# Performance work log

Hardware: AMD Instinct MI355X
Metric: run time of the kernel (lower is better)

## Reference

```python
import jax, jax.numpy as jnp
import numpy as np

B, C, H, W = 4, 2048, 32, 32


def conv1x1(x, Wt, b):
    # 1x1 conv == per-pixel matmul over channels
    return jnp.einsum('oc,bchw->bohw', Wt, x) + b[None, :, None, None]


def cross_attention(Q, K, V):
    b, c, h, w = Q.shape
    q = Q.reshape(b, c, h * w)   # [B, C, N]
    k = K.reshape(b, c, h * w)
    v = V.reshape(b, c, h * w)
    scores = jnp.einsum('bcn,bcm->bnm', q, k) / jnp.sqrt(jnp.asarray(c, jnp.float32))
    attn = jax.nn.softmax(scores, axis=-1)          # [B, N, N]
    out = jnp.einsum('bcm,bnm->bcn', v, attn)       # V @ attn^T
    return out.reshape(b, c, h, w)


def setup_inputs() -> dict:
    key = jax.random.key(0)
    ks = jax.random.split(key, 14)
    d = {
        'F_rgb': jax.random.normal(ks[0], (B, C, H, W), jnp.float32),
        'F_indices': jax.random.normal(ks[1], (B, C, H, W), jnp.float32),
    }
    names = ['q_rgb', 'k_rgb', 'v_rgb', 'q_ind', 'k_ind', 'v_ind']
    for i, n in enumerate(names):
        d['W_' + n] = jax.random.normal(ks[2 + 2 * i], (C, C), jnp.float32) * 0.02
        d['b_' + n] = jax.random.normal(ks[3 + 2 * i], (C,), jnp.float32) * 0.01
    return d


def reference(F_rgb, F_indices, W_q_rgb, b_q_rgb, W_k_rgb, b_k_rgb, W_v_rgb, b_v_rgb,
              W_q_ind, b_q_ind, W_k_ind, b_k_ind, W_v_ind, b_v_ind):
    # RGB queries attend over index features
    Q_rgb = conv1x1(F_rgb, W_q_rgb, b_q_rgb)
    K_ind = conv1x1(F_indices, W_k_ind, b_k_ind)
    V_ind = conv1x1(F_indices, W_v_ind, b_v_ind)
    F_rgb_attended = cross_attention(Q_rgb, K_ind, V_ind)
    # Index queries attend over RGB features
    Q_ind = conv1x1(F_indices, W_q_ind, b_q_ind)
    K_rgb = conv1x1(F_rgb, W_k_rgb, b_k_rgb)
    V_rgb = conv1x1(F_rgb, W_v_rgb, b_v_rgb)
    F_ind_attended = cross_attention(Q_ind, K_rgb, V_rgb)
    F_final = F_rgb_attended + F_ind_attended
    attention_weights = jnp.stack([F_rgb_attended, F_ind_attended], axis=1)  # [B,2,C,H,W]
    # pre_attention_outputs is an identity passthrough of the inputs
    return (F_final, F_rgb, F_indices, attention_weights)
```

## Files before the change

kernel.cpp:

```cpp
#include <hip/hip_runtime.h>

typedef __bf16 bf16x8 __attribute__((ext_vector_type(8)));
typedef float  f32x4  __attribute__((ext_vector_type(4)));
typedef unsigned short u16;
typedef unsigned short u16x8 __attribute__((ext_vector_type(8)));

__device__ __forceinline__ u16 f2bf(float f) {
  unsigned u = __builtin_bit_cast(unsigned, f);
  u += 0x7fffu + ((u >> 16) & 1u);
  return (u16)(u >> 16);
}
__device__ __forceinline__ float bf2f(u16 h) {
  return __builtin_bit_cast(float, (unsigned)h << 16);
}

using gvoid = __attribute__((address_space(1))) void;
using svoid = __attribute__((address_space(3))) void;
__device__ __forceinline__ void load_lds16(const void* g, void* s) {
  __builtin_amdgcn_global_load_lds((const gvoid*)g, (svoid*)s, 16, 0, 0);
}

__global__ void prep(const float* __restrict__ Fr, const float* __restrict__ Fi,
                     u16* __restrict__ FTr, u16* __restrict__ FTi,
                     float* __restrict__ Or, float* __restrict__ Oi,
                     const float* __restrict__ s0, const float* __restrict__ s1,
                     const float* __restrict__ s2, const float* __restrict__ s3,
                     const float* __restrict__ s4, const float* __restrict__ s5,
                     u16* __restrict__ Wall) {
  const int tx = threadIdx.x, ty = threadIdx.y;
  const int t2 = ty * 32 + tx;
  if (blockIdx.z >= 8) {
    const int gi = (blockIdx.z - 8) * 1024 + blockIdx.y * 32 + blockIdx.x;
    const int chunk = gi >> 12;
    const int i = (gi & 4095) * 256 + t2;
    const float* src;
    switch (chunk) {
      case 0: src = s0; break; case 1: src = s1; break; case 2: src = s2; break;
      case 3: src = s3; break; case 4: src = s4; break; default: src = s5; break;
    }
    float4 v = ((const float4*)src)[i];
    ushort4 o;
    o.x = f2bf(v.x); o.y = f2bf(v.y); o.z = f2bf(v.z); o.w = f2bf(v.w);
    ((ushort4*)(Wall + (long)chunk * 4194304))[i] = o;
    return;
  }
  __shared__ float tile[64][33];
  const int b = blockIdx.z & 3;
  const bool ind = (blockIdx.z >= 4);
  const float* F = ind ? Fi : Fr;
  u16* FT = ind ? FTi : FTr;
  float* O = ind ? Oi : Or;
  const int n0 = blockIdx.x * 32, c0 = blockIdx.y * 64;
  const long boff = (long)b * 2048 * 1024;
  const float* Fb = F + boff;
  float* Ob = O + boff;
  u16* FTb = FT + (long)b * 1024 * 2048;
#pragma unroll
  for (int i = 0; i < 8; ++i) {
    const long idx = (long)(c0 + ty + i * 8) * 1024 + n0 + tx;
    float v = Fb[idx];
    tile[ty + i * 8][tx] = v;
    Ob[idx] = v;
  }
  __syncthreads();
  const int q = t2 & 7, r = t2 >> 3;
  u16x8 o8;
#pragma unroll
  for (int k = 0; k < 8; ++k) o8[k] = f2bf(tile[8 * q + k][r]);
  *(u16x8*)(FTb + (long)(n0 + r) * 2048 + c0 + 8 * q) = o8;
}


#define BAR_ do { asm volatile("" ::: "memory"); __builtin_amdgcn_s_barrier(); \
                  asm volatile("" ::: "memory"); } while (0)
#define SB0 __builtin_amdgcn_sched_barrier(0)
#define LGK0 asm volatile("s_waitcnt lgkmcnt(0)" ::: "memory")
#define VMW6 asm volatile("s_waitcnt vmcnt(6)" ::: "memory")
#define VMW0 asm volatile("s_waitcnt vmcnt(0)" ::: "memory")

#define b0A0 0
#define b0A1 16384
#define b0B0 32768
#define b0B1 49152
#define b1A0 65536
#define b1A1 81920
#define b1B0 98304
#define b1B1 114688

#define STG(Mp, ld, row0, kt, off)                                                 \
  do {                                                                             \
    load_lds16(Mp + (long)((row0) + w * 8 + srow) * (ld) + (kt) * 64 + scol,       \
               sm + (off) + w * 1024);                                             \
    load_lds16(Mp + (long)((row0) + 64 + w * 8 + srow) * (ld) + (kt) * 64 + scol,  \
               sm + (off) + 8192 + w * 1024);                                      \
  } while (0)

#define RDA(off)                                                                   \
  _Pragma("unroll") for (int fm = 0; fm < 4; ++fm)                                 \
  _Pragma("unroll") for (int ks = 0; ks < 2; ++ks)                                 \
    fa[fm][ks] = *(const bf16x8*)(sm + (off) + aoff[fm] + kin[ks]);

#define RDB(off, dst)                                                              \
  _Pragma("unroll") for (int fn = 0; fn < 2; ++fn)                                 \
  _Pragma("unroll") for (int ks = 0; ks < 2; ++ks)                                 \
    dst[fn][ks] = *(const bf16x8*)(sm + (off) + boff[fn] + kin[ks]);

#define MMQ2(qa)                                                                   \
  __builtin_amdgcn_s_setprio(1);                                                   \
  _Pragma("unroll") for (int ks = 0; ks < 2; ++ks)                                 \
  _Pragma("unroll") for (int fm = 0; fm < 4; ++fm) {                               \
    _Pragma("unroll") for (int fn = 0; fn < 2; ++fn)                               \
      acc[qa][0][fm][fn] = __builtin_amdgcn_mfma_f32_16x16x32_bf16(                \
          fa[fm][ks], fb0[fn][ks], acc[qa][0][fm][fn], 0, 0, 0);                   \
    _Pragma("unroll") for (int fn = 0; fn < 2; ++fn)                               \
      acc[qa][1][fm][fn] = __builtin_amdgcn_mfma_f32_16x16x32_bf16(                \
          fa[fm][ks], fb1[fn][ks], acc[qa][1][fm][fn], 0, 0, 0);                   \
  }                                                                                \
  __builtin_amdgcn_s_setprio(0);

template <int OUT_BF16, int BIAS_MODE, int KSPLIT>
__global__ __launch_bounds__(512, 2) void gemm256(
    const u16* __restrict__ A0p, const u16* __restrict__ B0p, void* __restrict__ D0p,
    const float* __restrict__ ba0, const float* __restrict__ bb0,
    const u16* __restrict__ A1p, const u16* __restrict__ B1p, void* __restrict__ D1p,
    const float* __restrict__ ba1, const float* __restrict__ bb1,
    long sKH, int zsplit, int K, int lda, int ldb, int ldd,
    long sA, long sB, long sD) {
  __shared__ __attribute__((aligned(128))) char sm[131072];
  const int gx = gridDim.x, gy = gridDim.y;
  const int nwg = gx * gy * (int)gridDim.z;
  const int lin = blockIdx.x + gx * (blockIdx.y + gy * blockIdx.z);
  const int qch = nwg >> 3;
  int swzid = (lin & 7) * qch + (lin >> 3);
  const int bx = swzid % gx; swzid /= gx;
  const int by = swzid % gy;
  int zb = swzid / gy;
  int kh = 0;
  if (KSPLIT) { kh = zb >> 3; zb &= 7; }
  const bool s1 = (zb >= zsplit);
  const int zz = s1 ? zb - zsplit : zb;
  const u16* Ag = (s1 ? A1p : A0p) + (long)zz * sA + (long)kh * K;
  const u16* Bg = (s1 ? B1p : B0p) + (long)zz * sB + (long)kh * K;
  char* Dg = (char*)(s1 ? D1p : D0p) + (long)zz * sD * (OUT_BF16 ? 2 : 4)
           + (KSPLIT ? (long)kh * sKH : 0L);
  const float* ba = s1 ? ba1 : ba0;
  const float* bb = s1 ? bb1 : bb0;
  const int m0 = by * 256, n0 = bx * 256;
  const int t = threadIdx.x, w = t >> 6, l = t & 63;
  const int wr = w >> 2, wc = w & 3;
  const int lm = l & 15, lk = l >> 4;
  const int swz = (l & 7) << 4;
  const int srow = l >> 3;
  const int scol = ((l & 7) ^ srow) << 3;
  int aoff[4], boff[2], kin[2];
#pragma unroll
  for (int fm = 0; fm < 4; ++fm) aoff[fm] = (wr * 64 + fm * 16 + lm) * 128;
#pragma unroll
  for (int fn = 0; fn < 2; ++fn) boff[fn] = (wc * 32 + fn * 16 + lm) * 128;
  kin[0] = (lk * 16) ^ swz;
  kin[1] = (64 + lk * 16) ^ swz;

  f32x4 acc[2][2][4][2] = {};
  bf16x8 fa[4][2], fb0[2][2], fb1[2][2];

  const int nt = K >> 6;

  STG(Ag, lda, m0,       0, b0A0);
  STG(Bg, ldb, n0,       0, b0B0);
  STG(Bg, ldb, n0 + 128, 0, b0B1);
  STG(Ag, lda, m0 + 128, 0, b0A1);
  STG(Ag, lda, m0,       1, b1A0);
  STG(Bg, ldb, n0,       1, b1B0);
  STG(Bg, ldb, n0 + 128, 1, b1B1);
  VMW6;
  BAR_;

  for (int v = 0; v < nt; v += 2) {
    const int t2 = (v + 2 < nt) ? v + 2 : nt - 1;
    const int t3 = (v + 3 < nt) ? v + 3 : nt - 1;
    STG(Ag, lda, m0 + 128, v + 1, b1A1);
    RDA(b0A0); RDB(b0B0, fb0); RDB(b0B1, fb1);
    BAR_; LGK0; SB0; MMQ2(0);
    STG(Ag, lda, m0, t2, b0A0);
    STG(Bg, ldb, n0, t2, b0B0);
    STG(Bg, ldb, n0 + 128, t2, b0B1);
    RDA(b0A1);
    VMW6;
    BAR_; LGK0; SB0; MMQ2(1);
    STG(Ag, lda, m0 + 128, t2, b0A1);
    RDA(b1A0); RDB(b1B0, fb0); RDB(b1B1, fb1);
    BAR_; LGK0; SB0; MMQ2(0);
    STG(Ag, lda, m0, t3, b1A0);
    STG(Bg, ldb, n0, t3, b1B0);
    STG(Bg, ldb, n0 + 128, t3, b1B1);
    RDA(b1A1);
    VMW6;
    BAR_; LGK0; SB0; MMQ2(1);
  }

  VMW0;
  const int esz = OUT_BF16 ? 2 : 4;
#pragma unroll
  for (int qa = 0; qa < 2; ++qa)
#pragma unroll
    for (int fm = 0; fm < 4; ++fm) {
      BAR_;
#pragma unroll
      for (int qb = 0; qb < 2; ++qb)
#pragma unroll
        for (int fn = 0; fn < 2; ++fn) {
          const int col = qb * 128 + wc * 32 + fn * 16 + lm;
          const f32x4 vv = acc[qa][qb][fm][fn];
#pragma unroll
          for (int j = 0; j < 4; ++j) {
            const int r = wr * 16 + lk * 4 + j;
            float x = vv[j];
            if (BIAS_MODE == 1) {
              const int gc = n0 + col;
              x += (gc < 2048) ? ba[gc] : bb[gc - 2048];
            }
            if (BIAS_MODE == 2)
              x += ba[m0 + qa * 128 + wr * 64 + fm * 16 + lk * 4 + j];
            if (OUT_BF16) ((u16*)sm)[r * 256 + col] = f2bf(x);
            else          ((float*)sm)[r * 256 + col] = x;
          }
        }
      LGK0;
      BAR_;
#pragma unroll
      for (int p = 0; p < (OUT_BF16 ? 2 : 4); ++p) {
        const int off = p * 8192 + t * 16;
        const int r = OUT_BF16 ? (off >> 9) : (off >> 10);
        const int inrow = OUT_BF16 ? (off & 511) : (off & 1023);
        const int grow = m0 + qa * 128 + (r >> 4) * 64 + fm * 16 + (r & 15);
        const f32x4 d = *(const f32x4*)(sm + off);
        *(f32x4*)(Dg + ((long)grow * ldd + n0) * esz + inrow) = d;
      }
    }
}

__global__ void softmax_rows2(const u16* __restrict__ S0, const u16* __restrict__ S1,
                              u16* __restrict__ P, float alpha) {
  const long row = blockIdx.x;
  const int t = threadIdx.x, l = t & 63, w = t >> 6;
  ushort4 a = ((const ushort4*)(S0 + row * 1024))[t];
  ushort4 b = ((const ushort4*)(S1 + row * 1024))[t];
  float v0 = bf2f(a.x) + bf2f(b.x);
  float v1 = bf2f(a.y) + bf2f(b.y);
  float v2 = bf2f(a.z) + bf2f(b.z);
  float v3 = bf2f(a.w) + bf2f(b.w);
  __shared__ float red[8];
  float m = fmaxf(fmaxf(v0, v1), fmaxf(v2, v3));
#pragma unroll
  for (int off = 32; off; off >>= 1) m = fmaxf(m, __shfl_xor(m, off));
  if (l == 0) red[w] = m;
  __syncthreads();
  m = fmaxf(fmaxf(red[0], red[1]), fmaxf(red[2], red[3]));
  float e0 = __expf((v0 - m) * alpha);
  float e1 = __expf((v1 - m) * alpha);
  float e2 = __expf((v2 - m) * alpha);
  float e3 = __expf((v3 - m) * alpha);
  float s = e0 + e1 + e2 + e3;
#pragma unroll
  for (int off = 32; off; off >>= 1) s += __shfl_xor(s, off);
  if (l == 0) red[4 + w] = s;
  __syncthreads();
  s = red[4] + red[5] + red[6] + red[7];
  const float inv = 1.0f / s;
  ushort4 o;
  o.x = f2bf(e0 * inv); o.y = f2bf(e1 * inv);
  o.z = f2bf(e2 * inv); o.w = f2bf(e3 * inv);
  ((ushort4*)(P + row * 1024))[t] = o;
}

__global__ void final_add(const float4* __restrict__ aw, float4* __restrict__ dst) {
  const long i = (long)blockIdx.x * 256 + threadIdx.x;
  const long b = i >> 19;
  const long r = i & 524287;
  float4 a = aw[b * 1048576 + r];
  float4 c = aw[b * 1048576 + 524288 + r];
  float4 o;
  o.x = a.x + c.x; o.y = a.y + c.y; o.z = a.z + c.z; o.w = a.w + c.w;
  dst[i] = o;
}

extern "C" void kernel_launch(void* const* d_in, const int* in_sizes, int n_in,
                              void* d_out, int out_size, void* d_ws, size_t ws_size,
                              hipStream_t stream) {
  (void)in_sizes; (void)n_in; (void)out_size; (void)ws_size;
  const float* F_rgb = (const float*)d_in[0];
  const float* F_ind = (const float*)d_in[1];
  const float* bq_rgb = (const float*)d_in[3];
  const float* bk_rgb = (const float*)d_in[5];
  const float* bv_rgb = (const float*)d_in[7];
  const float* bq_ind = (const float*)d_in[9];
  const float* bk_ind = (const float*)d_in[11];
  const float* bv_ind = (const float*)d_in[13];

  char* ws = (char*)d_ws;
  u16* FT_rgb  = (u16*)(ws);
  u16* FT_ind  = (u16*)(ws + 16777216);
  u16* S1c     = (u16*)(ws);
  u16* Wall    = (u16*)(ws + 33554432);
  u16* Wqk_rgb = Wall;
  u16* Wqk_ind = (u16*)(ws + 50331648);
  u16* Wv_rgb  = (u16*)(ws + 67108864);
  u16* Wv_ind  = (u16*)(ws + 75497472);
  u16* QKT_rgb = (u16*)(ws + 83886080);
  u16* QKT_ind = (u16*)(ws + 117440512);
  u16* V_rgb   = (u16*)(ws + 150994944);
  u16* V_ind   = (u16*)(ws + 167772160);
  u16* S0c     = (u16*)(ws + 184549376);
  u16* P       = (u16*)(ws + 218103808);

  float* out       = (float*)d_out;
  float* out_final = out;
  float* out_Frgb  = out + 8388608;
  float* out_Find  = out + 16777216;
  float* AW        = out + 25165824;

  prep<<<dim3(32, 32, 32), dim3(32, 8), 0, stream>>>(
      F_rgb, F_ind, FT_rgb, FT_ind, out_Frgb, out_Find,
      (const float*)d_in[2], (const float*)d_in[4],
      (const float*)d_in[8], (const float*)d_in[10],
      (const float*)d_in[6], (const float*)d_in[12], Wall);

  gemm256<1, 1, 0><<<dim3(16, 4, 8), 512, 0, stream>>>(
      FT_rgb, Wqk_rgb, QKT_rgb, bq_rgb, bk_rgb,
      FT_ind, Wqk_ind, QKT_ind, bq_ind, bk_ind,
      0L, 4, 2048, 2048, 2048, 4096, 2097152L, 0L, 4194304L);

  gemm256<1, 2, 0><<<dim3(4, 8, 8), 512, 0, stream>>>(
      Wv_rgb, FT_rgb, V_rgb, bv_rgb, bv_rgb,
      Wv_ind, FT_ind, V_ind, bv_ind, bv_ind,
      0L, 4, 2048, 2048, 2048, 1024, 0L, 2097152L, 2097152L);

  gemm256<1, 0, 1><<<dim3(4, 4, 16), 512, 0, stream>>>(
      QKT_rgb, QKT_ind + 2048, S0c, nullptr, nullptr,
      QKT_ind, QKT_rgb + 2048, S0c + 4194304, nullptr, nullptr,
      (long)((char*)S1c - (char*)S0c), 4, 1024, 4096, 4096, 1024,
      4194304L, 4194304L, 1048576L);

  softmax_rows2<<<8192, 256, 0, stream>>>(S0c, S1c, P, 0.02209708691207961f);

  gemm256<0, 0, 0><<<dim3(4, 8, 8), 512, 0, stream>>>(
      V_ind, P, AW, nullptr, nullptr,
      V_rgb, P + 4194304, AW + 2097152, nullptr, nullptr,
      0L, 4, 1024, 1024, 1024, 1024, 2097152L, 1048576L, 4194304L);

  final_add<<<8192, 256, 0, stream>>>((const float4*)AW, (float4*)out_final);
}
```

Measured before the change: 325.4 us.

## Switch GEMMs to 256x128 tiles with K-step 32 for higher occupancy

Replaces the 256x256 GEMM tile (K-step 64, 128 KB LDS) with a 256x128 tile and K-step 32 using 48 KB LDS. Launch bounds rise to allow 4 blocks per CU, and grids double so each GEMM launches more workgroups. Staging, swizzling, wait counts and the epilogue are reworked for the new shape. This trades per-block data reuse and extra barriers per K for better CU fill and latency hiding.

```diff
diff --git a/kernel.cpp b/kernel.cpp
--- a/kernel.cpp
+++ b/kernel.cpp
@@ -75,58 +75,61 @@
                   asm volatile("" ::: "memory"); } while (0)
 #define SB0 __builtin_amdgcn_sched_barrier(0)
 #define LGK0 asm volatile("s_waitcnt lgkmcnt(0)" ::: "memory")
-#define VMW6 asm volatile("s_waitcnt vmcnt(6)" ::: "memory")
+#define VMW2 asm volatile("s_waitcnt vmcnt(2)" ::: "memory")
 #define VMW0 asm volatile("s_waitcnt vmcnt(0)" ::: "memory")
 
-#define b0A0 0
-#define b0A1 16384
-#define b0B0 32768
-#define b0B1 49152
-#define b1A0 65536
-#define b1A1 81920
-#define b1B0 98304
-#define b1B1 114688
+#define s0A0 0
+#define s0A1 8192
+#define s0B  16384
+#define s1A0 24576
+#define s1A1 32768
+#define s1B  40960
 
 #define STG(Mp, ld, row0, kt, off)                                                 \
-  do {                                                                             \
-    load_lds16(Mp + (long)((row0) + w * 8 + srow) * (ld) + (kt) * 64 + scol,       \
-               sm + (off) + w * 1024);                                             \
-    load_lds16(Mp + (long)((row0) + 64 + w * 8 + srow) * (ld) + (kt) * 64 + scol,  \
-               sm + (off) + 8192 + w * 1024);                                      \
-  } while (0)
-
-#define RDA(off)                                                                   \
+  load_lds16(Mp + (long)((row0) + srw) * (ld) + (kt) * 32 + scl,                   \
+             sm + (off) + w * 1024)
+
+#define RDA(bufA)                                                                  \
   _Pragma("unroll") for (int fm = 0; fm < 4; ++fm)                                 \
-  _Pragma("unroll") for (int ks = 0; ks < 2; ++ks)                                 \
-    fa[fm][ks] = *(const bf16x8*)(sm + (off) + aoff[fm] + kin[ks]);
-
-#define RDB(off, dst)                                                              \
+    fa[fm] = *(const bf16x8*)(sm + (bufA) + asel + aoff[fm] + kin32);
+
+#define RDBA(bufB)                                                                 \
   _Pragma("unroll") for (int fn = 0; fn < 2; ++fn)                                 \
-  _Pragma("unroll") for (int ks = 0; ks < 2; ++ks)                                 \
-    dst[fn][ks] = *(const bf16x8*)(sm + (off) + boff[fn] + kin[ks]);
-
-#define MMQ2(qa)                                                                   \
+    fbA[fn] = *(const bf16x8*)(sm + (bufB) + boff[fn] + kin32);
+
+#define RDBB(bufB)                                                                 \
+  _Pragma("unroll") for (int fn = 0; fn < 2; ++fn)                                 \
+    fbB[fn] = *(const bf16x8*)(sm + (bufB) + boff[2 + fn] + kin32);
+
+#define MMQA                                                                       \
   __builtin_amdgcn_s_setprio(1);                                                   \
-  _Pragma("unroll") for (int ks = 0; ks < 2; ++ks)                                 \
   _Pragma("unroll") for (int fm = 0; fm < 4; ++fm) {                               \
-    _Pragma("unroll") for (int fn = 0; fn < 2; ++fn)                               \
-      acc[qa][0][fm][fn] = __builtin_amdgcn_mfma_f32_16x16x32_bf16(                \
-          fa[fm][ks], fb0[fn][ks], acc[qa][0][fm][fn], 0, 0, 0);                   \
-    _Pragma("unroll") for (int fn = 0; fn < 2; ++fn)                               \
-      acc[qa][1][fm][fn] = __builtin_amdgcn_mfma_f32_16x16x32_bf16(                \
-          fa[fm][ks], fb1[fn][ks], acc[qa][1][fm][fn], 0, 0, 0);                   \
+    acc[fm][0] = __builtin_amdgcn_mfma_f32_16x16x32_bf16(fa[fm], fbA[0],           \
+                                                         acc[fm][0], 0, 0, 0);     \
+    acc[fm][1] = __builtin_amdgcn_mfma_f32_16x16x32_bf16(fa[fm], fbA[1],           \
+                                                         acc[fm][1], 0, 0, 0);     \
   }                                                                                \
   __builtin_amdgcn_s_setprio(0);
 
+#define MMQB                                                                       \
+  __builtin_amdgcn_s_setprio(1);                                                   \
+  _Pragma("unroll") for (int fm = 0; fm < 4; ++fm) {                               \
+    acc[fm][2] = __builtin_amdgcn_mfma_f32_16x16x32_bf16(fa[fm], fbB[0],           \
+                                                         acc[fm][2], 0, 0, 0);     \
+    acc[fm][3] = __builtin_amdgcn_mfma_f32_16x16x32_bf16(fa[fm], fbB[1],           \
+                                                         acc[fm][3], 0, 0, 0);     \
+  }                                                                                \
+  __builtin_amdgcn_s_setprio(0);
+
 template <int OUT_BF16, int BIAS_MODE, int KSPLIT>
-__global__ __launch_bounds__(512, 2) void gemm256(
+__global__ __launch_bounds__(512, 4) void gemm_tall(
     const u16* __restrict__ A0p, const u16* __restrict__ B0p, void* __restrict__ D0p,
     const float* __restrict__ ba0, const float* __restrict__ bb0,
     const u16* __restrict__ A1p, const u16* __restrict__ B1p, void* __restrict__ D1p,
     const float* __restrict__ ba1, const float* __restrict__ bb1,
     long sKH, int zsplit, int K, int lda, int ldb, int ldd,
     long sA, long sB, long sD) {
-  __shared__ __attribute__((aligned(128))) char sm[131072];
+  __shared__ __attribute__((aligned(128))) char sm[49152];
   const int gx = gridDim.x, gy = gridDim.y;
   const int nwg = gx * gy * (int)gridDim.z;
   const int lin = blockIdx.x + gx * (blockIdx.y + gy * blockIdx.z);
@@ -137,106 +140,97 @@
   int zb = swzid / gy;
   int kh = 0;
   if (KSPLIT) { kh = zb >> 3; zb &= 7; }
-  const bool s1 = (zb >= zsplit);
-  const int zz = s1 ? zb - zsplit : zb;
-  const u16* Ag = (s1 ? A1p : A0p) + (long)zz * sA + (long)kh * K;
-  const u16* Bg = (s1 ? B1p : B0p) + (long)zz * sB + (long)kh * K;
-  char* Dg = (char*)(s1 ? D1p : D0p) + (long)zz * sD * (OUT_BF16 ? 2 : 4)
+  const bool is1 = (zb >= zsplit);
+  const int zz = is1 ? zb - zsplit : zb;
+  const u16* Ag = (is1 ? A1p : A0p) + (long)zz * sA + (long)kh * K;
+  const u16* Bg = (is1 ? B1p : B0p) + (long)zz * sB + (long)kh * K;
+  char* Dg = (char*)(is1 ? D1p : D0p) + (long)zz * sD * (OUT_BF16 ? 2 : 4)
            + (KSPLIT ? (long)kh * sKH : 0L);
-  const float* ba = s1 ? ba1 : ba0;
-  const float* bb = s1 ? bb1 : bb0;
-  const int m0 = by * 256, n0 = bx * 256;
+  const float* ba = is1 ? ba1 : ba0;
+  const float* bb = is1 ? bb1 : bb0;
+  const int m0 = by * 256, n0 = bx * 128;
   const int t = threadIdx.x, w = t >> 6, l = t & 63;
-  const int wr = w >> 2, wc = w & 3;
+  const int wr = w >> 1, wc = w & 1;
   const int lm = l & 15, lk = l >> 4;
-  const int swz = (l & 7) << 4;
-  const int srow = l >> 3;
-  const int scol = ((l & 7) ^ srow) << 3;
-  int aoff[4], boff[2], kin[2];
-#pragma unroll
-  for (int fm = 0; fm < 4; ++fm) aoff[fm] = (wr * 64 + fm * 16 + lm) * 128;
-#pragma unroll
-  for (int fn = 0; fn < 2; ++fn) boff[fn] = (wc * 32 + fn * 16 + lm) * 128;
-  kin[0] = (lk * 16) ^ swz;
-  kin[1] = (64 + lk * 16) ^ swz;
-
-  f32x4 acc[2][2][4][2] = {};
-  bf16x8 fa[4][2], fb0[2][2], fb1[2][2];
-
-  const int nt = K >> 6;
-
-  STG(Ag, lda, m0,       0, b0A0);
-  STG(Bg, ldb, n0,       0, b0B0);
-  STG(Bg, ldb, n0 + 128, 0, b0B1);
-  STG(Ag, lda, m0 + 128, 0, b0A1);
-  STG(Ag, lda, m0,       1, b1A0);
-  STG(Bg, ldb, n0,       1, b1B0);
-  STG(Bg, ldb, n0 + 128, 1, b1B1);
-  VMW6;
+  const int srw = (w << 4) + (l >> 2);
+  const int scl = (((l & 3) ^ ((l >> 2) & 3)) << 3);
+  const int asel = (wr >= 2) ? 8192 : 0;
+  const int kin32 = ((lk ^ (lm & 3)) << 4);
+  int aoff[4], boff[4];
+#pragma unroll
+  for (int fm = 0; fm < 4; ++fm) aoff[fm] = ((wr & 1) * 64 + fm * 16 + lm) * 64;
+#pragma unroll
+  for (int fn = 0; fn < 4; ++fn) boff[fn] = (wc * 64 + fn * 16 + lm) * 64;
+
+  f32x4 acc[4][4] = {};
+  bf16x8 fa[4], fbA[2], fbB[2];
+
+  const int nt = K >> 5;
+
+  STG(Ag, lda, m0,       0, s0A0);
+  STG(Ag, lda, m0 + 128, 0, s0A1);
+  STG(Bg, ldb, n0,       0, s0B);
+  STG(Ag, lda, m0,       1, s1A0);
+  STG(Ag, lda, m0 + 128, 1, s1A1);
+  VMW2;
   BAR_;
 
   for (int v = 0; v < nt; v += 2) {
     const int t2 = (v + 2 < nt) ? v + 2 : nt - 1;
     const int t3 = (v + 3 < nt) ? v + 3 : nt - 1;
-    STG(Ag, lda, m0 + 128, v + 1, b1A1);
-    RDA(b0A0); RDB(b0B0, fb0); RDB(b0B1, fb1);
-    BAR_; LGK0; SB0; MMQ2(0);
-    STG(Ag, lda, m0, t2, b0A0);
-    STG(Bg, ldb, n0, t2, b0B0);
-    STG(Bg, ldb, n0 + 128, t2, b0B1);
-    RDA(b0A1);
-    VMW6;
-    BAR_; LGK0; SB0; MMQ2(1);
-    STG(Ag, lda, m0 + 128, t2, b0A1);
-    RDA(b1A0); RDB(b1B0, fb0); RDB(b1B1, fb1);
-    BAR_; LGK0; SB0; MMQ2(0);
-    STG(Ag, lda, m0, t3, b1A0);
-    STG(Bg, ldb, n0, t3, b1B0);
-    STG(Bg, ldb, n0 + 128, t3, b1B1);
-    RDA(b1A1);
-    VMW6;
-    BAR_; LGK0; SB0; MMQ2(1);
+    STG(Bg, ldb, n0, v + 1, s1B);
+    RDA(s0A0); RDBA(s0B);
+    BAR_; LGK0; SB0; MMQA;
+    STG(Ag, lda, m0,       t2, s0A0);
+    STG(Ag, lda, m0 + 128, t2, s0A1);
+    RDBB(s0B);
+    VMW2;
+    BAR_; LGK0; SB0; MMQB;
+    STG(Bg, ldb, n0, t2, s0B);
+    RDA(s1A0); RDBA(s1B);
+    BAR_; LGK0; SB0; MMQA;
+    STG(Ag, lda, m0,       t3, s1A0);
+    STG(Ag, lda, m0 + 128, t3, s1A1);
+    RDBB(s1B);
+    VMW2;
+    BAR_; LGK0; SB0; MMQB;
   }
 
   VMW0;
   const int esz = OUT_BF16 ? 2 : 4;
 #pragma unroll
-  for (int qa = 0; qa < 2; ++qa)
-#pragma unroll
-    for (int fm = 0; fm < 4; ++fm) {
-      BAR_;
-#pragma unroll
-      for (int qb = 0; qb < 2; ++qb)
-#pragma unroll
-        for (int fn = 0; fn < 2; ++fn) {
-          const int col = qb * 128 + wc * 32 + fn * 16 + lm;
-          const f32x4 vv = acc[qa][qb][fm][fn];
-#pragma unroll
-          for (int j = 0; j < 4; ++j) {
-            const int r = wr * 16 + lk * 4 + j;
-            float x = vv[j];
-            if (BIAS_MODE == 1) {
-              const int gc = n0 + col;
-              x += (gc < 2048) ? ba[gc] : bb[gc - 2048];
-            }
-            if (BIAS_MODE == 2)
-              x += ba[m0 + qa * 128 + wr * 64 + fm * 16 + lk * 4 + j];
-            if (OUT_BF16) ((u16*)sm)[r * 256 + col] = f2bf(x);
-            else          ((float*)sm)[r * 256 + col] = x;
-          }
+  for (int fm = 0; fm < 4; ++fm) {
+    BAR_;
+#pragma unroll
+    for (int fn = 0; fn < 4; ++fn) {
+      const int col = wc * 64 + fn * 16 + lm;
+      const f32x4 vv = acc[fm][fn];
+#pragma unroll
+      for (int j = 0; j < 4; ++j) {
+        const int r = wr * 16 + lk * 4 + j;
+        float x = vv[j];
+        if (BIAS_MODE == 1) {
+          const int gc = n0 + col;
+          x += (gc < 2048) ? ba[gc] : bb[gc - 2048];
         }
-      LGK0;
-      BAR_;
-#pragma unroll
-      for (int p = 0; p < (OUT_BF16 ? 2 : 4); ++p) {
-        const int off = p * 8192 + t * 16;
-        const int r = OUT_BF16 ? (off >> 9) : (off >> 10);
-        const int inrow = OUT_BF16 ? (off & 511) : (off & 1023);
-        const int grow = m0 + qa * 128 + (r >> 4) * 64 + fm * 16 + (r & 15);
-        const f32x4 d = *(const f32x4*)(sm + off);
-        *(f32x4*)(Dg + ((long)grow * ldd + n0) * esz + inrow) = d;
+        if (BIAS_MODE == 2)
+          x += ba[m0 + wr * 64 + fm * 16 + lk * 4 + j];
+        if (OUT_BF16) ((u16*)sm)[r * 128 + col] = f2bf(x);
+        else          ((float*)sm)[r * 128 + col] = x;
       }
     }
+    LGK0;
+    BAR_;
+#pragma unroll
+    for (int p = 0; p < (OUT_BF16 ? 2 : 4); ++p) {
+      const int off = p * 8192 + t * 16;
+      const int r = OUT_BF16 ? (off >> 8) : (off >> 9);
+      const int inrow = OUT_BF16 ? (off & 255) : (off & 511);
+      const int grow = m0 + (r >> 4) * 64 + fm * 16 + (r & 15);
+      const f32x4 d = *(const f32x4*)(sm + off);
+      *(f32x4*)(Dg + ((long)grow * ldd + n0) * esz + inrow) = d;
+    }
+  }
 }
 
 __global__ void softmax_rows2(const u16* __restrict__ S0, const u16* __restrict__ S1,
@@ -325,17 +319,17 @@
       (const float*)d_in[8], (const float*)d_in[10],
       (const float*)d_in[6], (const float*)d_in[12], Wall);
 
-  gemm256<1, 1, 0><<<dim3(16, 4, 8), 512, 0, stream>>>(
+  gemm_tall<1, 1, 0><<<dim3(32, 4, 8), 512, 0, stream>>>(
       FT_rgb, Wqk_rgb, QKT_rgb, bq_rgb, bk_rgb,
       FT_ind, Wqk_ind, QKT_ind, bq_ind, bk_ind,
       0L, 4, 2048, 2048, 2048, 4096, 2097152L, 0L, 4194304L);
 
-  gemm256<1, 2, 0><<<dim3(4, 8, 8), 512, 0, stream>>>(
+  gemm_tall<1, 2, 0><<<dim3(8, 8, 8), 512, 0, stream>>>(
       Wv_rgb, FT_rgb, V_rgb, bv_rgb, bv_rgb,
       Wv_ind, FT_ind, V_ind, bv_ind, bv_ind,
       0L, 4, 2048, 2048, 2048, 1024, 0L, 2097152L, 2097152L);
 
-  gemm256<1, 0, 1><<<dim3(4, 4, 16), 512, 0, stream>>>(
+  gemm_tall<1, 0, 1><<<dim3(8, 4, 16), 512, 0, stream>>>(
       QKT_rgb, QKT_ind + 2048, S0c, nullptr, nullptr,
       QKT_ind, QKT_rgb + 2048, S0c + 4194304, nullptr, nullptr,
       (long)((char*)S1c - (char*)S0c), 4, 1024, 4096, 4096, 1024,
@@ -343,7 +337,7 @@
 
   softmax_rows2<<<8192, 256, 0, stream>>>(S0c, S1c, P, 0.02209708691207961f);
 
-  gemm256<0, 0, 0><<<dim3(4, 8, 8), 512, 0, stream>>>(
+  gemm_tall<0, 0, 0><<<dim3(8, 8, 8), 512, 0, stream>>>(
       V_ind, P, AW, nullptr, nullptr,
       V_rgb, P + 4194304, AW + 2097152, nullptr, nullptr,
       0L, 4, 1024, 1024, 1024, 1024, 2097152L, 1048576L, 4194304L);
```

After: 374.6 us. 1.15x slower.
